# Kernel optimization log

Hardware: AMD Instinct MI355X
Metric: run time of the kernel (lower is better)

The kernel has to match this reference:

```python
import jax, jax.numpy as jnp
import numpy as np

N, H, W, SD = 64, 22, 22, 8
HW = H * W


def _conv(x, w, b):
    # 3x3 SAME conv, NCHW / OIHW
    y = jax.lax.conv_general_dilated(x, w, (1, 1), 'SAME',
                                     dimension_numbers=('NCHW', 'OIHW', 'NCHW'))
    return y + b[None, :, None, None]


def _bn(x, g, b, eps=1e-5):
    # BatchNorm2d in training mode: batch statistics over (N, H, W)
    m = jnp.mean(x, axis=(0, 2, 3), keepdims=True)
    v = jnp.var(x, axis=(0, 2, 3), keepdims=True)
    return (x - m) * jax.lax.rsqrt(v + eps) * g[None, :, None, None] + b[None, :, None, None]


def setup_inputs() -> dict:
    key = jax.random.key(0)
    ks = iter(jax.random.split(key, 64))
    def kw(shape):  # kaiming-normal fan_in init
        fan_in = int(np.prod(shape[1:]))
        return jax.random.normal(next(ks), shape, jnp.float32) * np.float32(np.sqrt(2.0 / fan_in))
    d = {
        'cost_volume': jax.random.normal(next(ks), (N, HW, H, W), jnp.float32),
        'state_prev': jax.random.normal(next(ks), (N, SD, H, W), jnp.float32),
        'dimp_score_cur': jax.random.normal(next(ks), (N, 1, H, W), jnp.float32),
    }
    for p in ('cv1', 'cv2'):  # two cost-volume processing stacks: conv(1->8)+BN+ReLU, conv(8->1)+BN
        d[p + '_w1'] = kw((8, 1, 3, 3)); d[p + '_b1'] = jnp.zeros(8, jnp.float32)
        d[p + '_g1'] = jnp.ones(8, jnp.float32); d[p + '_be1'] = jnp.zeros(8, jnp.float32)
        d[p + '_w2'] = kw((1, 8, 3, 3)); d[p + '_b2'] = jnp.zeros(1, jnp.float32)
        d[p + '_g2'] = jnp.ones(1, jnp.float32); d[p + '_be2'] = jnp.zeros(1, jnp.float32)
    d['rp1_w'] = kw((64, SD + 2, 3, 3)); d['rp1_b'] = jnp.zeros(64, jnp.float32)
    d['rp2_w'] = kw((32, 64, 3, 3)); d['rp2_b'] = jnp.zeros(32, jnp.float32)
    d['resp_w'] = kw((1, 32, 3, 3)); d['resp_b'] = jnp.zeros(1, jnp.float32)
    for g_ in ('gru_r', 'gru_u', 'gru_o'):  # ConvGRUCell(input=4, hidden=SD, ksz=3)
        d[g_ + 'w'] = kw((SD, 4 + SD, 3, 3)); d[g_ + 'b'] = jnp.zeros(SD, jnp.float32)
    return d


def _fwd(cost_volume, state_prev, dimp_score_cur,
         cv1_w1, cv1_b1, cv1_g1, cv1_be1, cv1_w2, cv1_b2, cv1_g2, cv1_be2,
         cv2_w1, cv2_b1, cv2_g1, cv2_be1, cv2_w2, cv2_b2, cv2_g2, cv2_be2,
         rp1_w, rp1_b, rp2_w, rp2_b, resp_w, resp_b,
         gru_rw, gru_rb, gru_uw, gru_ub, gru_ow, gru_ob):
    n = cost_volume.shape[0]
    # ---- cost volume processing 1: per-map spatial softmax ----
    x = cost_volume.reshape(-1, 1, H, W)                       # (N*HW, 1, H, W)
    p = jax.nn.relu(_bn(_conv(x, cv1_w1, cv1_b1), cv1_g1, cv1_be1))
    p = _bn(_conv(p, cv1_w2, cv1_b2), cv1_g2, cv1_be2)
    p = jax.nn.softmax(p.reshape(-1, HW), axis=1).reshape(-1, 1, H, W)
    # ---- cost volume processing 2: softmax over source positions ----
    p = jax.nn.relu(_bn(_conv(p, cv2_w1, cv2_b1), cv2_g1, cv2_be1))
    p = _bn(_conv(p, cv2_w2, cv2_b2), cv2_g2, cv2_be2)
    p = jax.nn.softmax(p.reshape(n, HW, H, W), axis=1)         # propagation weights (n, p, h, w)
    # ---- confidence ('max') ----
    conf = jnp.max(p, axis=1, keepdims=True)                   # (N, 1, H, W)
    # ---- state propagation: contract over source positions (no (N,HW,C,H,W) intermediate) ----
    s = state_prev.transpose(0, 2, 3, 1).reshape(n, HW, SD)    # (n, p, d)
    prop_h = jnp.einsum('nphw,npd->ndhw', p, s)                # (N, SD, H, W)
    # ---- response prediction ----
    pin = jnp.concatenate([prop_h, dimp_score_cur, conf], axis=1)   # (N, SD+2, H, W)
    r = jax.nn.relu(_conv(pin, rp1_w, rp1_b))
    r = jax.nn.relu(_conv(r, rp2_w, rp2_b))
    fused = jax.nn.sigmoid(_conv(r, resp_w, resp_b))           # (N, 1, H, W)
    # ---- ConvGRU state update ----
    scores_cat = jnp.concatenate([dimp_score_cur, fused], axis=1)   # (N, 2, H, W)
    pool = jnp.max(scores_cat, axis=(2, 3), keepdims=True)          # adaptive max pool to 1x1
    gin = jnp.concatenate([scores_cat, jnp.broadcast_to(pool, scores_cat.shape)], axis=1)  # (N,4,H,W)
    stacked = jnp.concatenate([gin, prop_h], axis=1)           # (N, 4+SD, H, W)
    upd = jax.nn.sigmoid(_conv(stacked, gru_uw, gru_ub))
    rst = jax.nn.sigmoid(_conv(stacked, gru_rw, gru_rb))
    out = jnp.tanh(_conv(jnp.concatenate([gin, prop_h * rst], axis=1), gru_ow, gru_ob))
    state_new = prop_h * (1.0 - upd) + out * upd               # (N, SD, H, W)
    return jnp.concatenate([fused, state_new], axis=1)         # (N, 1+SD, H, W)


def reference(cost_volume, state_prev, dimp_score_cur,
              cv1_w1, cv1_b1, cv1_g1, cv1_be1, cv1_w2, cv1_b2, cv1_g2, cv1_be2,
              cv2_w1, cv2_b1, cv2_g1, cv2_be1, cv2_w2, cv2_b2, cv2_g2, cv2_be2,
              rp1_w, rp1_b, rp2_w, rp2_b, resp_w, resp_b,
              gru_rw, gru_rb, gru_uw, gru_ub, gru_ow, gru_ob):
    return _fwd(cost_volume, state_prev, dimp_score_cur,
                cv1_w1, cv1_b1, cv1_g1, cv1_be1, cv1_w2, cv1_b2, cv1_g2, cv1_be2,
                cv2_w1, cv2_b1, cv2_g1, cv2_be1, cv2_w2, cv2_b2, cv2_g2, cv2_be2,
                rp1_w, rp1_b, rp2_w, rp2_b, resp_w, resp_b,
                gru_rw, gru_rb, gru_uw, gru_ub, gru_ow, gru_ob)
```

## Files before the change

kernel.cpp:

```cpp
#include <hip/hip_runtime.h>

#define HH 22
#define WW 22
#define HWN 484
#define NBATCH 64
#define SDIM 8
#define NMAPS (NBATCH*HWN)
#define PADW 24
#define PADSZ (PADW*PADW)
#define INVC (1.f/14992384.f)

#define LD12(A,b0) \
    float t00=(A)[(b0)],        t01=(A)[(b0)+1],        t02=(A)[(b0)+2], \
          t10=(A)[(b0)+PADW],   t11=(A)[(b0)+PADW+1],   t12=(A)[(b0)+PADW+2], \
          t20=(A)[(b0)+2*PADW], t21=(A)[(b0)+2*PADW+1], t22=(A)[(b0)+2*PADW+2], \
          t30=(A)[(b0)+3*PADW], t31=(A)[(b0)+3*PADW+1], t32=(A)[(b0)+3*PADW+2]

#define DOT9(w9,a0,a1,a2,b0_,b1_,b2_,c0,c1,c2,init) \
    fmaf((w9)[0],a0,fmaf((w9)[1],a1,fmaf((w9)[2],a2, \
    fmaf((w9)[3],b0_,fmaf((w9)[4],b1_,fmaf((w9)[5],b2_, \
    fmaf((w9)[6],c0,fmaf((w9)[7],c1,fmaf((w9)[8],c2,(init))))))))))

#define LOAD_NB(arr, bb) do { \
    nb[0]=(arr)[(bb)-PADW-1]; nb[1]=(arr)[(bb)-PADW]; nb[2]=(arr)[(bb)-PADW+1]; \
    nb[3]=(arr)[(bb)-1];      nb[4]=(arr)[(bb)];      nb[5]=(arr)[(bb)+1]; \
    nb[6]=(arr)[(bb)+PADW-1]; nb[7]=(arr)[(bb)+PADW]; nb[8]=(arr)[(bb)+PADW+1]; } while(0)

__global__ __launch_bounds__(256) void k_stats(const float* __restrict__ src,
    const float* __restrict__ w, const float* __restrict__ b,
    float* __restrict__ Sg, float* __restrict__ Qg)
{
    __shared__ float xin[PADSZ];
    __shared__ float red[16];
    int tid=threadIdx.x;
    for(int q=tid;q<PADSZ;q+=256) xin[q]=0.f;
    float accS[8], accQ[8];
#pragma unroll
    for(int c=0;c<8;++c){ accS[c]=0.f; accQ[c]=0.f; }
    bool act = tid<242;
    int i2 = tid/22, jj = tid - i2*22;
    int b0 = 2*i2*PADW + jj;
    int m0=blockIdx.x*16;
    for(int m=m0;m<m0+16;++m){
        __syncthreads();
        const float* sp = src + (size_t)m*HWN;
        { int p=tid;     int i=p/22, j=p-i*22; xin[(i+1)*PADW+j+1]=sp[p]; }
        { int p=tid+256; if(p<HWN){ int i=p/22, j=p-i*22; xin[(i+1)*PADW+j+1]=sp[p]; } }
        __syncthreads();
        if(act){
            LD12(xin,b0);
#pragma unroll
            for(int c=0;c<8;++c){
                const float* w9=w+c*9;
                float bc=b[c];
                float y0=DOT9(w9,t00,t01,t02,t10,t11,t12,t20,t21,t22,bc);
                float y1=DOT9(w9,t10,t11,t12,t20,t21,t22,t30,t31,t32,bc);
                accS[c]+=y0+y1;
                accQ[c]=fmaf(y0,y0,accQ[c]); accQ[c]=fmaf(y1,y1,accQ[c]);
            }
        }
    }
    __syncthreads();
    if(tid<16) red[tid]=0.f;
    __syncthreads();
#pragma unroll
    for(int c=0;c<8;++c){
        float s=accS[c], q=accQ[c];
        for(int o=32;o;o>>=1){ s+=__shfl_down(s,o); q+=__shfl_down(q,o); }
        if((tid&63)==0){ atomicAdd(&red[c],s); atomicAdd(&red[8+c],q); }
    }
    __syncthreads();
    if(tid<8){ atomicAdd(&Sg[tid],red[tid]); atomicAdd(&Qg[tid],red[8+tid]); }
}

__global__ __launch_bounds__(256) void k_convpair(const float* __restrict__ src, float* __restrict__ Ydst,
    const float* __restrict__ w1, const float* __restrict__ b1,
    const float* __restrict__ Sin, const float* __restrict__ Qin,
    const float* __restrict__ g, const float* __restrict__ be,
    const float* __restrict__ w2, const float* __restrict__ b2,
    float* __restrict__ Sg, float* __restrict__ Qg)
{
    __shared__ float xin[PADSZ];
    __shared__ float z[8*PADSZ];
    __shared__ float red[2];
    __shared__ float scs[8], shs[8];
    int tid=threadIdx.x;
    if(tid<8){
        float mean=Sin[tid]*INVC;
        float var=fmaf(-mean,mean,Qin[tid]*INVC);
        float sc=g[tid]*rsqrtf(var+1e-5f);
        scs[tid]=sc; shs[tid]=fmaf(-mean,sc,be[tid]);
    }
    for(int q=tid;q<PADSZ;q+=256) xin[q]=0.f;
    for(int q=tid;q<8*PADSZ;q+=256) z[q]=0.f;
    float aS=0.f, aQ=0.f;
    bool act = tid<242;
    int i2 = tid/22, jj = tid - i2*22;
    int b0 = 2*i2*PADW + jj;
    int zb = b0 + PADW + 1;
    int ptop = 2*i2*22 + jj;
    float b2v=b2[0];
    int m0=blockIdx.x*16;
    for(int m=m0;m<m0+16;++m){
        __syncthreads();
        const float* sp = src + (size_t)m*HWN;
        { int p=tid;     int i=p/22, j=p-i*22; xin[(i+1)*PADW+j+1]=sp[p]; }
        { int p=tid+256; if(p<HWN){ int i=p/22, j=p-i*22; xin[(i+1)*PADW+j+1]=sp[p]; } }
        __syncthreads();
        if(act){
            LD12(xin,b0);
#pragma unroll
            for(int c=0;c<8;++c){
                const float* w9=w1+c*9;
                float bc=b1[c], sc=scs[c], sh=shs[c];
                float y0=DOT9(w9,t00,t01,t02,t10,t11,t12,t20,t21,t22,bc);
                float y1=DOT9(w9,t10,t11,t12,t20,t21,t22,t30,t31,t32,bc);
                y0=fmaf(y0,sc,sh); y1=fmaf(y1,sc,sh);
                z[c*PADSZ+zb]      = y0>0.f?y0:0.f;
                z[c*PADSZ+zb+PADW] = y1>0.f?y1:0.f;
            }
        }
        __syncthreads();
        if(act){
            float y0=b2v, y1=b2v;
#pragma unroll
            for(int c=0;c<8;++c){
                const float* w9=w2+c*9;
                int cb=c*PADSZ+b0;
                LD12(z,cb);
                y0=DOT9(w9,t00,t01,t02,t10,t11,t12,t20,t21,t22,y0);
                y1=DOT9(w9,t10,t11,t12,t20,t21,t22,t30,t31,t32,y1);
            }
            float* yp = Ydst + (size_t)m*HWN;
            yp[ptop]=y0; yp[ptop+22]=y1;
            aS+=y0+y1; aQ=fmaf(y0,y0,aQ); aQ=fmaf(y1,y1,aQ);
        }
    }
    __syncthreads();
    if(tid<2) red[tid]=0.f;
    __syncthreads();
    for(int o=32;o;o>>=1){ aS+=__shfl_down(aS,o); aQ+=__shfl_down(aQ,o); }
    if((tid&63)==0){ atomicAdd(&red[0],aS); atomicAdd(&red[1],aQ); }
    __syncthreads();
    if(tid==0){ atomicAdd(Sg,red[0]); atomicAdd(Qg,red[1]); }
}

__global__ __launch_bounds__(256) void k_smax_stats(float* __restrict__ Y,
    const float* __restrict__ S2, const float* __restrict__ Q2,
    const float* __restrict__ g2, const float* __restrict__ be2,
    const float* __restrict__ w, const float* __restrict__ b,
    float* __restrict__ Sg, float* __restrict__ Qg)
{
    __shared__ float xin[PADSZ];
    __shared__ float red4[4];
    __shared__ float red[16];
    int tid=threadIdx.x;
    float mean=S2[0]*INVC;
    float var=fmaf(-mean,mean,Q2[0]*INVC);
    float a=g2[0]*rsqrtf(var+1e-5f);
    float sh=fmaf(-mean,a,be2[0]);
    for(int q=tid;q<PADSZ;q+=256) xin[q]=0.f;
    float accS[8], accQ[8];
#pragma unroll
    for(int c=0;c<8;++c){ accS[c]=0.f; accQ[c]=0.f; }
    bool act = tid<242;
    int i2 = tid/22, jj = tid - i2*22;
    int b0 = 2*i2*PADW + jj;
    int p0=tid, p1=tid+256;
    int i0=p0/22, j0=p0-i0*22; int aa0=(i0+1)*PADW+j0+1;
    int aa1=0; if(p1<HWN){ int i1=p1/22, j1=p1-i1*22; aa1=(i1+1)*PADW+j1+1; }
    int m0=blockIdx.x*16;
    for(int m=m0;m<m0+16;++m){
        __syncthreads();
        float* yp = Y + (size_t)m*HWN;
        float e0=__expf(fmaf(yp[p0],a,sh)); xin[aa0]=e0;
        float e1=0.f;
        if(p1<HWN){ e1=__expf(fmaf(yp[p1],a,sh)); xin[aa1]=e1; }
        float part=e0+e1;
        for(int o=32;o;o>>=1) part+=__shfl_down(part,o);
        if((tid&63)==0) red4[tid>>6]=part;
        __syncthreads();
        float inv=1.f/(red4[0]+red4[1]+red4[2]+red4[3]);
        yp[p0]=e0*inv;
        if(p1<HWN) yp[p1]=e1*inv;
        if(act){
            LD12(xin,b0);
#pragma unroll
            for(int c=0;c<8;++c){
                const float* w9=w+c*9;
                float d0=DOT9(w9,t00,t01,t02,t10,t11,t12,t20,t21,t22,0.f);
                float d1=DOT9(w9,t10,t11,t12,t20,t21,t22,t30,t31,t32,0.f);
                float y0=fmaf(inv,d0,b[c]);
                float y1=fmaf(inv,d1,b[c]);
                accS[c]+=y0+y1;
                accQ[c]=fmaf(y0,y0,accQ[c]); accQ[c]=fmaf(y1,y1,accQ[c]);
            }
        }
    }
    __syncthreads();
    if(tid<16) red[tid]=0.f;
    __syncthreads();
#pragma unroll
    for(int c=0;c<8;++c){
        float s=accS[c], q=accQ[c];
        for(int o=32;o;o>>=1){ s+=__shfl_down(s,o); q+=__shfl_down(q,o); }
        if((tid&63)==0){ atomicAdd(&red[c],s); atomicAdd(&red[8+c],q); }
    }
    __syncthreads();
    if(tid<8){ atomicAdd(&Sg[tid],red[tid]); atomicAdd(&Qg[tid],red[8+tid]); }
}

__global__ __launch_bounds__(128) void k_prop(const float* __restrict__ Y,
    const float* __restrict__ S4, const float* __restrict__ Q4,
    const float* __restrict__ g4, const float* __restrict__ be4,
    const float* __restrict__ state, float* __restrict__ prop, float* __restrict__ conf)
{
    int n=blockIdx.x;
    __shared__ float sst[8*HWN];
    int tid=threadIdx.x;
    for(int q=tid;q<8*HWN;q+=128) sst[q]=state[(size_t)n*8*HWN + q];
    __syncthreads();
    int t = blockIdx.y*121 + tid;
    if(tid>=121) return;
    float mean=S4[0]*INVC;
    float var=fmaf(-mean,mean,Q4[0]*INVC);
    float a=g4[0]*rsqrtf(var+1e-5f);
    float sh=fmaf(-mean,a,be4[0]);
    const float* col = Y + (size_t)n*HWN*HWN + t;
    float mx=-1e30f, ssum=0.f;
    float acc[8];
#pragma unroll
    for(int d=0;d<8;++d) acc[d]=0.f;
#pragma unroll 4
    for(int p=0;p<HWN;++p){
        float v=fmaf(col[(size_t)p*HWN], a, sh);
        float e=__expf(v);
        mx=fmaxf(mx,v);
        ssum+=e;
#pragma unroll
        for(int d=0;d<8;++d) acc[d]=fmaf(e, sst[d*HWN+p], acc[d]);
    }
    float inv=1.f/ssum;
    conf[(size_t)n*HWN+t]=__expf(mx)*inv;
#pragma unroll
    for(int d=0;d<8;++d) prop[((size_t)n*8+d)*HWN+t]=acc[d]*inv;
}

__global__ __launch_bounds__(256) void k_rp1(const float* __restrict__ prop,
    const float* __restrict__ dimp, const float* __restrict__ conf,
    const float* __restrict__ wf, const float* __restrict__ bfv, float* __restrict__ R1)
{
    int n=blockIdx.x, g=blockIdx.y;
    __shared__ float pin[10*PADSZ];
    int tid=threadIdx.x;
    for(int i=tid;i<10*PADSZ;i+=256) pin[i]=0.f;
    __syncthreads();
    for(int p=tid;p<HWN;p+=256){
        int i=p/WW, j=p-i*WW; int aa=(i+1)*PADW+j+1;
#pragma unroll
        for(int d=0;d<8;++d) pin[d*PADSZ+aa]=prop[((size_t)n*8+d)*HWN+p];
        pin[8*PADSZ+aa]=dimp[(size_t)n*HWN+p];
        pin[9*PADSZ+aa]=conf[(size_t)n*HWN+p];
    }
    __syncthreads();
    const float* wg = wf + (size_t)(g*16)*90;
    for(int p=tid;p<HWN;p+=256){
        int i=p/WW, j=p-i*WW; int aa=(i+1)*PADW+j+1;
        float acc[16];
#pragma unroll
        for(int o=0;o<16;++o) acc[o]=bfv[g*16+o];
#pragma unroll
        for(int c=0;c<10;++c){
            float nb[9]; int bb=c*PADSZ+aa;
            LOAD_NB(pin, bb);
#pragma unroll
            for(int o=0;o<16;++o){
                const float* w=wg+o*90+c*9;
#pragma unroll
                for(int t=0;t<9;++t) acc[o]=fmaf(w[t], nb[t], acc[o]);
            }
        }
#pragma unroll
        for(int o=0;o<16;++o){
            float y=acc[o];
            R1[((size_t)n*64 + g*16+o)*HWN+p]= y>0.f?y:0.f;
        }
    }
}

__global__ __launch_bounds__(512) void k_rp2(const float* __restrict__ R1,
    const float* __restrict__ wf, const float* __restrict__ bfv, float* __restrict__ R2)
{
    int n=blockIdx.x, g=blockIdx.y;
    __shared__ float xc[16*PADSZ];
    int tid=threadIdx.x;
    for(int i=tid;i<16*PADSZ;i+=512) xc[i]=0.f;
    int p=tid; bool act = p<HWN;
    int i=p/WW, j=p-i*WW, aa=(i+1)*PADW+j+1;
    float acc[8];
#pragma unroll
    for(int o=0;o<8;++o) acc[o]=0.f;
    for(int k=0;k<4;++k){
        __syncthreads();
        for(int q=tid;q<16*HWN;q+=512){
            int ic=q/HWN, pp=q-ic*HWN;
            int ii=pp/WW, jj=pp-ii*WW;
            xc[ic*PADSZ+(ii+1)*PADW+jj+1]=R1[((size_t)n*64 + k*16+ic)*HWN+pp];
        }
        __syncthreads();
        if(act){
#pragma unroll
            for(int ic=0;ic<16;++ic){
                float nb[9]; int bb=ic*PADSZ+aa;
                LOAD_NB(xc, bb);
#pragma unroll
                for(int o=0;o<8;++o){
                    const float* w = wf + ((size_t)(g*8+o)*64 + k*16+ic)*9;
#pragma unroll
                    for(int t=0;t<9;++t) acc[o]=fmaf(w[t], nb[t], acc[o]);
                }
            }
        }
    }
    if(act){
#pragma unroll
        for(int o=0;o<8;++o){
            float y=acc[o]+bfv[g*8+o];
            R2[((size_t)n*32+g*8+o)*HWN+p]= y>0.f?y:0.f;
        }
    }
}

__global__ __launch_bounds__(512) void k_resp(const float* __restrict__ R2,
    const float* __restrict__ wf, const float* __restrict__ bfv,
    const float* __restrict__ dimp, float* __restrict__ fused,
    float* __restrict__ pool, float* __restrict__ out)
{
    int n=blockIdx.x;
    __shared__ float xc[16*PADSZ];
    __shared__ float redf[8], redd[8];
    int tid=threadIdx.x;
    for(int i=tid;i<16*PADSZ;i+=512) xc[i]=0.f;
    int p=tid; bool act=p<HWN;
    int i=p/WW, j=p-i*WW, aa=(i+1)*PADW+j+1;
    float acc=0.f;
    for(int k=0;k<2;++k){
        __syncthreads();
        for(int q=tid;q<16*HWN;q+=512){
            int ic=q/HWN, pp=q-ic*HWN;
            int ii=pp/WW, jj=pp-ii*WW;
            xc[ic*PADSZ+(ii+1)*PADW+jj+1]=R2[((size_t)n*32+k*16+ic)*HWN+pp];
        }
        __syncthreads();
        if(act){
#pragma unroll
            for(int ic=0;ic<16;++ic){
                float nb[9]; int bb=ic*PADSZ+aa;
                LOAD_NB(xc, bb);
                const float* w=wf+(size_t)(k*16+ic)*9;
#pragma unroll
                for(int t=0;t<9;++t) acc=fmaf(w[t], nb[t], acc);
            }
        }
    }
    float fval=-1e30f, dval=-1e30f;
    if(act){
        float y=acc+bfv[0];
        float s=1.f/(1.f+__expf(-y));
        fused[(size_t)n*HWN+p]=s;
        out[(size_t)n*9*HWN+p]=s;
        fval=s;
        dval=dimp[(size_t)n*HWN+p];
    }
    int lane=tid&63, wid=tid>>6;
    for(int o=32;o;o>>=1){ fval=fmaxf(fval,__shfl_xor(fval,o)); dval=fmaxf(dval,__shfl_xor(dval,o)); }
    if(lane==0){ redf[wid]=fval; redd[wid]=dval; }
    __syncthreads();
    if(tid==0){
        float fm=redf[0], dm=redd[0];
        for(int q=1;q<8;++q){ fm=fmaxf(fm,redf[q]); dm=fmaxf(dm,redd[q]); }
        pool[n*2+0]=dm; pool[n*2+1]=fm;
    }
}

__global__ __launch_bounds__(512) void k_gru(const float* __restrict__ dimp,
    const float* __restrict__ fused, const float* __restrict__ pool,
    const float* __restrict__ prop,
    const float* __restrict__ wr, const float* __restrict__ br,
    const float* __restrict__ wu, const float* __restrict__ bu,
    const float* __restrict__ wo, const float* __restrict__ bo,
    float* __restrict__ out)
{
    int n=blockIdx.x;
    __shared__ float sg[12*PADSZ];
    __shared__ float pr[8*PADSZ];
    int tid=threadIdx.x;
    for(int i=tid;i<12*PADSZ;i+=512) sg[i]=0.f;
    for(int i=tid;i<8*PADSZ;i+=512) pr[i]=0.f;
    __syncthreads();
    float p0=pool[n*2+0], p1=pool[n*2+1];
    for(int p=tid;p<HWN;p+=512){
        int i=p/WW, j=p-i*WW, aa=(i+1)*PADW+j+1;
        sg[0*PADSZ+aa]=dimp[(size_t)n*HWN+p];
        sg[1*PADSZ+aa]=fused[(size_t)n*HWN+p];
        sg[2*PADSZ+aa]=p0;
        sg[3*PADSZ+aa]=p1;
#pragma unroll
        for(int d=0;d<8;++d) sg[(4+d)*PADSZ+aa]=prop[((size_t)n*8+d)*HWN+p];
    }
    __syncthreads();
    int p=tid; bool act=p<HWN;
    int i=p/WW, j=p-i*WW, aa=(i+1)*PADW+j+1;
    float upd[8];
    if(act){
        float ua[8], ra[8];
#pragma unroll
        for(int o=0;o<8;++o){ ua[o]=bu[o]; ra[o]=br[o]; }
#pragma unroll
        for(int ic=0;ic<12;++ic){
            float nb[9]; int bb=ic*PADSZ+aa;
            LOAD_NB(sg, bb);
#pragma unroll
            for(int o=0;o<8;++o){
                const float* wup=wu+((size_t)o*12+ic)*9;
                const float* wrp=wr+((size_t)o*12+ic)*9;
#pragma unroll
                for(int t=0;t<9;++t){
                    ua[o]=fmaf(wup[t], nb[t], ua[o]);
                    ra[o]=fmaf(wrp[t], nb[t], ra[o]);
                }
            }
        }
#pragma unroll
        for(int o=0;o<8;++o){
            upd[o]=1.f/(1.f+__expf(-ua[o]));
            float rst=1.f/(1.f+__expf(-ra[o]));
            pr[o*PADSZ+aa]=sg[(4+o)*PADSZ+aa]*rst;
        }
    }
    __syncthreads();
    if(act){
        float oa[8];
#pragma unroll
        for(int o=0;o<8;++o) oa[o]=bo[o];
#pragma unroll
        for(int ic=0;ic<12;++ic){
            const float* srcp = (ic<4)? (sg+ic*PADSZ) : (pr+(ic-4)*PADSZ);
            float nb[9]; int bb=aa;
            LOAD_NB(srcp, bb);
#pragma unroll
            for(int o=0;o<8;++o){
                const float* wop=wo+((size_t)o*12+ic)*9;
#pragma unroll
                for(int t=0;t<9;++t) oa[o]=fmaf(wop[t], nb[t], oa[o]);
            }
        }
#pragma unroll
        for(int o=0;o<8;++o){
            float od=tanhf(oa[o]);
            float ph=sg[(4+o)*PADSZ+aa];
            float sn=ph*(1.f-upd[o])+od*upd[o];
            out[((size_t)n*9+1+o)*HWN+p]=sn;
        }
    }
}

extern "C" void kernel_launch(void* const* d_in, const int* in_sizes, int n_in,
                              void* d_out, int out_size, void* d_ws, size_t ws_size,
                              hipStream_t stream)
{
    (void)in_sizes; (void)n_in; (void)out_size; (void)ws_size;
    float* ws=(float*)d_ws;
    float* Y     = ws;
    float* PROP  = ws + 14992384;
    float* CONF  = PROP + 247808;
    float* FUSED = CONF + 30976;
    float* POOL  = FUSED + 30976;
    float* STATS = POOL + 128;
    float* R1    = ws;
    float* R2    = ws + 4000000;

    const float* cv    = (const float*)d_in[0];
    const float* state = (const float*)d_in[1];
    const float* dimp  = (const float*)d_in[2];
    float* out = (float*)d_out;

    hipMemsetAsync(STATS, 0, 36*sizeof(float), stream);

    float *S1=STATS,*Q1=STATS+8,*S2=STATS+16,*Q2=STATS+17,*S3=STATS+18,*Q3=STATS+26,*S4=STATS+34,*Q4=STATS+35;

    const float* cv1_w1=(const float*)d_in[3];  const float* cv1_b1=(const float*)d_in[4];
    const float* cv1_g1=(const float*)d_in[5];  const float* cv1_be1=(const float*)d_in[6];
    const float* cv1_w2=(const float*)d_in[7];  const float* cv1_b2=(const float*)d_in[8];
    const float* cv1_g2=(const float*)d_in[9];  const float* cv1_be2=(const float*)d_in[10];
    const float* cv2_w1=(const float*)d_in[11]; const float* cv2_b1=(const float*)d_in[12];
    const float* cv2_g1=(const float*)d_in[13]; const float* cv2_be1=(const float*)d_in[14];
    const float* cv2_w2=(const float*)d_in[15]; const float* cv2_b2=(const float*)d_in[16];
    const float* cv2_g2=(const float*)d_in[17]; const float* cv2_be2=(const float*)d_in[18];
    const float* rp1_w=(const float*)d_in[19];  const float* rp1_b=(const float*)d_in[20];
    const float* rp2_w=(const float*)d_in[21];  const float* rp2_b=(const float*)d_in[22];
    const float* resp_w=(const float*)d_in[23]; const float* resp_b=(const float*)d_in[24];
    const float* gru_rw=(const float*)d_in[25]; const float* gru_rb=(const float*)d_in[26];
    const float* gru_uw=(const float*)d_in[27]; const float* gru_ub=(const float*)d_in[28];
    const float* gru_ow=(const float*)d_in[29]; const float* gru_ob=(const float*)d_in[30];

    k_stats<<<1936,256,0,stream>>>(cv, cv1_w1, cv1_b1, S1, Q1);
    k_convpair<<<1936,256,0,stream>>>(cv, Y, cv1_w1, cv1_b1, S1, Q1, cv1_g1, cv1_be1,
                                      cv1_w2, cv1_b2, S2, Q2);
    k_smax_stats<<<1936,256,0,stream>>>(Y, S2, Q2, cv1_g2, cv1_be2, cv2_w1, cv2_b1, S3, Q3);
    k_convpair<<<1936,256,0,stream>>>(Y, Y, cv2_w1, cv2_b1, S3, Q3, cv2_g1, cv2_be1,
                                      cv2_w2, cv2_b2, S4, Q4);
    k_prop<<<dim3(64,4),128,0,stream>>>(Y, S4, Q4, cv2_g2, cv2_be2, state, PROP, CONF);
    k_rp1<<<dim3(64,4),256,0,stream>>>(PROP, dimp, CONF, rp1_w, rp1_b, R1);
    k_rp2<<<dim3(64,4),512,0,stream>>>(R1, rp2_w, rp2_b, R2);
    k_resp<<<64,512,0,stream>>>(R2, resp_w, resp_b, dimp, FUSED, POOL, out);
    k_gru<<<64,512,0,stream>>>(dimp, FUSED, POOL, PROP,
                               gru_rw, gru_rb, gru_uw, gru_ub, gru_ow, gru_ob, out);
}
```

Baseline: 849.4 us.

## Map one thread per padded cell, double-buffer map loads, split prop reduction

```diff
diff --git a/kernel.cpp b/kernel.cpp
--- a/kernel.cpp
+++ b/kernel.cpp
@@ -6,61 +6,57 @@
 #define NBATCH 64
 #define SDIM 8
 #define NMAPS (NBATCH*HWN)
+#define PW 24
+#define CELLS 576
 #define PADW 24
 #define PADSZ (PADW*PADW)
 #define INVC (1.f/14992384.f)
 
-#define LD12(A,b0) \
-    float t00=(A)[(b0)],        t01=(A)[(b0)+1],        t02=(A)[(b0)+2], \
-          t10=(A)[(b0)+PADW],   t11=(A)[(b0)+PADW+1],   t12=(A)[(b0)+PADW+2], \
-          t20=(A)[(b0)+2*PADW], t21=(A)[(b0)+2*PADW+1], t22=(A)[(b0)+2*PADW+2], \
-          t30=(A)[(b0)+3*PADW], t31=(A)[(b0)+3*PADW+1], t32=(A)[(b0)+3*PADW+2]
-
-#define DOT9(w9,a0,a1,a2,b0_,b1_,b2_,c0,c1,c2,init) \
-    fmaf((w9)[0],a0,fmaf((w9)[1],a1,fmaf((w9)[2],a2, \
-    fmaf((w9)[3],b0_,fmaf((w9)[4],b1_,fmaf((w9)[5],b2_, \
-    fmaf((w9)[6],c0,fmaf((w9)[7],c1,fmaf((w9)[8],c2,(init))))))))))
+#define LD9(A, idx) \
+  float x0=(A)[(idx)-PW-1], x1=(A)[(idx)-PW], x2=(A)[(idx)-PW+1], \
+        x3=(A)[(idx)-1],    x4=(A)[(idx)],    x5=(A)[(idx)+1], \
+        x6=(A)[(idx)+PW-1], x7=(A)[(idx)+PW], x8=(A)[(idx)+PW+1]
+#define DOT9W(w9, init) \
+  fmaf((w9)[0],x0,fmaf((w9)[1],x1,fmaf((w9)[2],x2,fmaf((w9)[3],x3,fmaf((w9)[4],x4, \
+  fmaf((w9)[5],x5,fmaf((w9)[6],x6,fmaf((w9)[7],x7,fmaf((w9)[8],x8,(init))))))))))
 
 #define LOAD_NB(arr, bb) do { \
     nb[0]=(arr)[(bb)-PADW-1]; nb[1]=(arr)[(bb)-PADW]; nb[2]=(arr)[(bb)-PADW+1]; \
     nb[3]=(arr)[(bb)-1];      nb[4]=(arr)[(bb)];      nb[5]=(arr)[(bb)+1]; \
     nb[6]=(arr)[(bb)+PADW-1]; nb[7]=(arr)[(bb)+PADW]; nb[8]=(arr)[(bb)+PADW+1]; } while(0)
 
-__global__ __launch_bounds__(256) void k_stats(const float* __restrict__ src,
+__global__ __launch_bounds__(576) void k_stats(const float* __restrict__ src,
     const float* __restrict__ w, const float* __restrict__ b,
     float* __restrict__ Sg, float* __restrict__ Qg)
 {
-    __shared__ float xin[PADSZ];
+    __shared__ float xin[2][CELLS];
     __shared__ float red[16];
     int tid=threadIdx.x;
-    for(int q=tid;q<PADSZ;q+=256) xin[q]=0.f;
+    int i=tid/PW, j=tid-i*PW;
+    bool inter = (i>=1 && i<=22 && j>=1 && j<=22);
+    int p=(i-1)*22+(j-1);
+    xin[0][tid]=0.f; xin[1][tid]=0.f;
     float accS[8], accQ[8];
 #pragma unroll
     for(int c=0;c<8;++c){ accS[c]=0.f; accQ[c]=0.f; }
-    bool act = tid<242;
-    int i2 = tid/22, jj = tid - i2*22;
-    int b0 = 2*i2*PADW + jj;
     int m0=blockIdx.x*16;
-    for(int m=m0;m<m0+16;++m){
-        __syncthreads();
-        const float* sp = src + (size_t)m*HWN;
-        { int p=tid;     int i=p/22, j=p-i*22; xin[(i+1)*PADW+j+1]=sp[p]; }
-        { int p=tid+256; if(p<HWN){ int i=p/22, j=p-i*22; xin[(i+1)*PADW+j+1]=sp[p]; } }
-        __syncthreads();
-        if(act){
-            LD12(xin,b0);
+    if(inter) xin[0][tid]=src[(size_t)m0*HWN+p];
+    __syncthreads();
+    for(int mi=0;mi<16;++mi){
+        int cur=mi&1;
+        float nx=0.f;
+        if(mi<15 && inter) nx=src[(size_t)(m0+mi+1)*HWN+p];
+        if(inter){
+            LD9(xin[cur], tid);
 #pragma unroll
             for(int c=0;c<8;++c){
-                const float* w9=w+c*9;
-                float bc=b[c];
-                float y0=DOT9(w9,t00,t01,t02,t10,t11,t12,t20,t21,t22,bc);
-                float y1=DOT9(w9,t10,t11,t12,t20,t21,t22,t30,t31,t32,bc);
-                accS[c]+=y0+y1;
-                accQ[c]=fmaf(y0,y0,accQ[c]); accQ[c]=fmaf(y1,y1,accQ[c]);
-            }
-        }
-    }
-    __syncthreads();
+                float y=DOT9W(w+c*9, b[c]);
+                accS[c]+=y; accQ[c]=fmaf(y,y,accQ[c]);
+            }
+        }
+        if(mi<15 && inter) xin[cur^1][tid]=nx;
+        __syncthreads();
+    }
     if(tid<16) red[tid]=0.f;
     __syncthreads();
 #pragma unroll
@@ -73,70 +69,62 @@
     if(tid<8){ atomicAdd(&Sg[tid],red[tid]); atomicAdd(&Qg[tid],red[8+tid]); }
 }
 
-__global__ __launch_bounds__(256) void k_convpair(const float* __restrict__ src, float* __restrict__ Ydst,
+__global__ __launch_bounds__(576) void k_convpair(const float* __restrict__ src, float* __restrict__ Ydst,
     const float* __restrict__ w1, const float* __restrict__ b1,
     const float* __restrict__ Sin, const float* __restrict__ Qin,
     const float* __restrict__ g, const float* __restrict__ be,
     const float* __restrict__ w2, const float* __restrict__ b2,
     float* __restrict__ Sg, float* __restrict__ Qg)
 {
-    __shared__ float xin[PADSZ];
-    __shared__ float z[8*PADSZ];
+    __shared__ float xin[2][CELLS];
+    __shared__ float z[8][CELLS];
+    __shared__ float scs[8], shs[8];
     __shared__ float red[2];
-    __shared__ float scs[8], shs[8];
-    int tid=threadIdx.x;
+    int tid=threadIdx.x;
+    int i=tid/PW, j=tid-i*PW;
+    bool inter = (i>=1 && i<=22 && j>=1 && j<=22);
+    int p=(i-1)*22+(j-1);
+    xin[0][tid]=0.f; xin[1][tid]=0.f;
+#pragma unroll
+    for(int c=0;c<8;++c) z[c][tid]=0.f;
     if(tid<8){
         float mean=Sin[tid]*INVC;
         float var=fmaf(-mean,mean,Qin[tid]*INVC);
         float sc=g[tid]*rsqrtf(var+1e-5f);
         scs[tid]=sc; shs[tid]=fmaf(-mean,sc,be[tid]);
     }
-    for(int q=tid;q<PADSZ;q+=256) xin[q]=0.f;
-    for(int q=tid;q<8*PADSZ;q+=256) z[q]=0.f;
     float aS=0.f, aQ=0.f;
-    bool act = tid<242;
-    int i2 = tid/22, jj = tid - i2*22;
-    int b0 = 2*i2*PADW + jj;
-    int zb = b0 + PADW + 1;
-    int ptop = 2*i2*22 + jj;
     float b2v=b2[0];
     int m0=blockIdx.x*16;
-    for(int m=m0;m<m0+16;++m){
-        __syncthreads();
-        const float* sp = src + (size_t)m*HWN;
-        { int p=tid;     int i=p/22, j=p-i*22; xin[(i+1)*PADW+j+1]=sp[p]; }
-        { int p=tid+256; if(p<HWN){ int i=p/22, j=p-i*22; xin[(i+1)*PADW+j+1]=sp[p]; } }
-        __syncthreads();
-        if(act){
-            LD12(xin,b0);
+    if(inter) xin[0][tid]=src[(size_t)m0*HWN+p];
+    __syncthreads();
+    for(int mi=0;mi<16;++mi){
+        int cur=mi&1;
+        float nx=0.f;
+        if(mi<15 && inter) nx=src[(size_t)(m0+mi+1)*HWN+p];
+        if(inter){
+            LD9(xin[cur], tid);
 #pragma unroll
             for(int c=0;c<8;++c){
-                const float* w9=w1+c*9;
-                float bc=b1[c], sc=scs[c], sh=shs[c];
-                float y0=DOT9(w9,t00,t01,t02,t10,t11,t12,t20,t21,t22,bc);
-                float y1=DOT9(w9,t10,t11,t12,t20,t21,t22,t30,t31,t32,bc);
-                y0=fmaf(y0,sc,sh); y1=fmaf(y1,sc,sh);
-                z[c*PADSZ+zb]      = y0>0.f?y0:0.f;
-                z[c*PADSZ+zb+PADW] = y1>0.f?y1:0.f;
-            }
-        }
-        __syncthreads();
-        if(act){
-            float y0=b2v, y1=b2v;
+                float y=DOT9W(w1+c*9, b1[c]);
+                y=fmaf(y,scs[c],shs[c]);
+                z[c][tid]=y>0.f?y:0.f;
+            }
+        }
+        if(mi<15 && inter) xin[cur^1][tid]=nx;
+        __syncthreads();
+        if(inter){
+            float y=b2v;
 #pragma unroll
             for(int c=0;c<8;++c){
-                const float* w9=w2+c*9;
-                int cb=c*PADSZ+b0;
-                LD12(z,cb);
-                y0=DOT9(w9,t00,t01,t02,t10,t11,t12,t20,t21,t22,y0);
-                y1=DOT9(w9,t10,t11,t12,t20,t21,t22,t30,t31,t32,y1);
-            }
-            float* yp = Ydst + (size_t)m*HWN;
-            yp[ptop]=y0; yp[ptop+22]=y1;
-            aS+=y0+y1; aQ=fmaf(y0,y0,aQ); aQ=fmaf(y1,y1,aQ);
-        }
-    }
-    __syncthreads();
+                LD9(z[c], tid);
+                y=DOT9W(w2+c*9, y);
+            }
+            Ydst[(size_t)(m0+mi)*HWN+p]=y;
+            aS+=y; aQ=fmaf(y,y,aQ);
+        }
+        __syncthreads();
+    }
     if(tid<2) red[tid]=0.f;
     __syncthreads();
     for(int o=32;o;o>>=1){ aS+=__shfl_down(aS,o); aQ+=__shfl_down(aQ,o); }
@@ -145,59 +133,50 @@
     if(tid==0){ atomicAdd(Sg,red[0]); atomicAdd(Qg,red[1]); }
 }
 
-__global__ __launch_bounds__(256) void k_smax_stats(float* __restrict__ Y,
+__global__ __launch_bounds__(576) void k_smax_stats(float* __restrict__ Y,
     const float* __restrict__ S2, const float* __restrict__ Q2,
     const float* __restrict__ g2, const float* __restrict__ be2,
     const float* __restrict__ w, const float* __restrict__ b,
     float* __restrict__ Sg, float* __restrict__ Qg)
 {
-    __shared__ float xin[PADSZ];
-    __shared__ float red4[4];
+    __shared__ float xin[CELLS];
+    __shared__ float red9[9];
     __shared__ float red[16];
     int tid=threadIdx.x;
+    int i=tid/PW, j=tid-i*PW;
+    bool inter = (i>=1 && i<=22 && j>=1 && j<=22);
+    int p=(i-1)*22+(j-1);
     float mean=S2[0]*INVC;
     float var=fmaf(-mean,mean,Q2[0]*INVC);
     float a=g2[0]*rsqrtf(var+1e-5f);
     float sh=fmaf(-mean,a,be2[0]);
-    for(int q=tid;q<PADSZ;q+=256) xin[q]=0.f;
+    xin[tid]=0.f;
     float accS[8], accQ[8];
 #pragma unroll
     for(int c=0;c<8;++c){ accS[c]=0.f; accQ[c]=0.f; }
-    bool act = tid<242;
-    int i2 = tid/22, jj = tid - i2*22;
-    int b0 = 2*i2*PADW + jj;
-    int p0=tid, p1=tid+256;
-    int i0=p0/22, j0=p0-i0*22; int aa0=(i0+1)*PADW+j0+1;
-    int aa1=0; if(p1<HWN){ int i1=p1/22, j1=p1-i1*22; aa1=(i1+1)*PADW+j1+1; }
     int m0=blockIdx.x*16;
-    for(int m=m0;m<m0+16;++m){
-        __syncthreads();
-        float* yp = Y + (size_t)m*HWN;
-        float e0=__expf(fmaf(yp[p0],a,sh)); xin[aa0]=e0;
-        float e1=0.f;
-        if(p1<HWN){ e1=__expf(fmaf(yp[p1],a,sh)); xin[aa1]=e1; }
-        float part=e0+e1;
+    for(int mi=0;mi<16;++mi){
+        size_t off=(size_t)(m0+mi)*HWN+p;
+        float e = inter ? __expf(fmaf(Y[off],a,sh)) : 0.f;
+        float part=e;
         for(int o=32;o;o>>=1) part+=__shfl_down(part,o);
-        if((tid&63)==0) red4[tid>>6]=part;
-        __syncthreads();
-        float inv=1.f/(red4[0]+red4[1]+red4[2]+red4[3]);
-        yp[p0]=e0*inv;
-        if(p1<HWN) yp[p1]=e1*inv;
-        if(act){
-            LD12(xin,b0);
+        if((tid&63)==0) red9[tid>>6]=part;
+        xin[tid]=e;
+        __syncthreads();
+        float sum=red9[0]+red9[1]+red9[2]+red9[3]+red9[4]+red9[5]+red9[6]+red9[7]+red9[8];
+        float inv=1.f/sum;
+        if(inter){
+            Y[off]=e*inv;
+            LD9(xin, tid);
 #pragma unroll
             for(int c=0;c<8;++c){
-                const float* w9=w+c*9;
-                float d0=DOT9(w9,t00,t01,t02,t10,t11,t12,t20,t21,t22,0.f);
-                float d1=DOT9(w9,t10,t11,t12,t20,t21,t22,t30,t31,t32,0.f);
-                float y0=fmaf(inv,d0,b[c]);
-                float y1=fmaf(inv,d1,b[c]);
-                accS[c]+=y0+y1;
-                accQ[c]=fmaf(y0,y0,accQ[c]); accQ[c]=fmaf(y1,y1,accQ[c]);
-            }
-        }
-    }
-    __syncthreads();
+                float d=DOT9W(w+c*9, 0.f);
+                float y=fmaf(inv,d,b[c]);
+                accS[c]+=y; accQ[c]=fmaf(y,y,accQ[c]);
+            }
+        }
+        __syncthreads();
+    }
     if(tid<16) red[tid]=0.f;
     __syncthreads();
 #pragma unroll
@@ -210,40 +189,54 @@
     if(tid<8){ atomicAdd(&Sg[tid],red[tid]); atomicAdd(&Qg[tid],red[8+tid]); }
 }
 
-__global__ __launch_bounds__(128) void k_prop(const float* __restrict__ Y,
+__global__ __launch_bounds__(512) void k_prop(const float* __restrict__ Y,
     const float* __restrict__ S4, const float* __restrict__ Q4,
     const float* __restrict__ g4, const float* __restrict__ be4,
     const float* __restrict__ state, float* __restrict__ prop, float* __restrict__ conf)
 {
     int n=blockIdx.x;
     __shared__ float sst[8*HWN];
-    int tid=threadIdx.x;
-    for(int q=tid;q<8*HWN;q+=128) sst[q]=state[(size_t)n*8*HWN + q];
-    __syncthreads();
-    int t = blockIdx.y*121 + tid;
-    if(tid>=121) return;
+    __shared__ float part[4][121][10];
+    int tid=threadIdx.x;
+    for(int q=tid;q<8*HWN;q+=512) sst[q]=state[(size_t)n*8*HWN + q];
+    __syncthreads();
+    int tq=tid&127, pc=tid>>7;
+    int t=blockIdx.y*121+tq;
     float mean=S4[0]*INVC;
     float var=fmaf(-mean,mean,Q4[0]*INVC);
     float a=g4[0]*rsqrtf(var+1e-5f);
     float sh=fmaf(-mean,a,be4[0]);
-    const float* col = Y + (size_t)n*HWN*HWN + t;
-    float mx=-1e30f, ssum=0.f;
-    float acc[8];
-#pragma unroll
-    for(int d=0;d<8;++d) acc[d]=0.f;
+    if(tq<121){
+        const float* col = Y + (size_t)n*HWN*HWN + t + (size_t)pc*121*HWN;
+        const float* sp = sst + pc*121;
+        float mx=-1e30f, ssum=0.f;
+        float acc[8];
+#pragma unroll
+        for(int d=0;d<8;++d) acc[d]=0.f;
 #pragma unroll 4
-    for(int p=0;p<HWN;++p){
-        float v=fmaf(col[(size_t)p*HWN], a, sh);
-        float e=__expf(v);
-        mx=fmaxf(mx,v);
-        ssum+=e;
-#pragma unroll
-        for(int d=0;d<8;++d) acc[d]=fmaf(e, sst[d*HWN+p], acc[d]);
-    }
-    float inv=1.f/ssum;
-    conf[(size_t)n*HWN+t]=__expf(mx)*inv;
-#pragma unroll
-    for(int d=0;d<8;++d) prop[((size_t)n*8+d)*HWN+t]=acc[d]*inv;
+        for(int p=0;p<121;++p){
+            float v=fmaf(col[(size_t)p*HWN], a, sh);
+            float e=__expf(v);
+            mx=fmaxf(mx,v); ssum+=e;
+#pragma unroll
+            for(int d=0;d<8;++d) acc[d]=fmaf(e, sp[d*HWN+p], acc[d]);
+        }
+        part[pc][tq][0]=ssum; part[pc][tq][1]=mx;
+#pragma unroll
+        for(int d=0;d<8;++d) part[pc][tq][2+d]=acc[d];
+    }
+    __syncthreads();
+    if(pc==0 && tq<121){
+        float ssum=part[0][tq][0]+part[1][tq][0]+part[2][tq][0]+part[3][tq][0];
+        float mx=fmaxf(fmaxf(part[0][tq][1],part[1][tq][1]),fmaxf(part[2][tq][1],part[3][tq][1]));
+        float inv=1.f/ssum;
+        conf[(size_t)n*HWN+t]=__expf(mx)*inv;
+#pragma unroll
+        for(int d=0;d<8;++d){
+            float acd=part[0][tq][2+d]+part[1][tq][2+d]+part[2][tq][2+d]+part[3][tq][2+d];
+            prop[((size_t)n*8+d)*HWN+t]=acd*inv;
+        }
+    }
 }
 
 __global__ __launch_bounds__(256) void k_rp1(const float* __restrict__ prop,
@@ -504,13 +497,13 @@
     const float* gru_uw=(const float*)d_in[27]; const float* gru_ub=(const float*)d_in[28];
     const float* gru_ow=(const float*)d_in[29]; const float* gru_ob=(const float*)d_in[30];
 
-    k_stats<<<1936,256,0,stream>>>(cv, cv1_w1, cv1_b1, S1, Q1);
-    k_convpair<<<1936,256,0,stream>>>(cv, Y, cv1_w1, cv1_b1, S1, Q1, cv1_g1, cv1_be1,
+    k_stats<<<1936,576,0,stream>>>(cv, cv1_w1, cv1_b1, S1, Q1);
+    k_convpair<<<1936,576,0,stream>>>(cv, Y, cv1_w1, cv1_b1, S1, Q1, cv1_g1, cv1_be1,
                                       cv1_w2, cv1_b2, S2, Q2);
-    k_smax_stats<<<1936,256,0,stream>>>(Y, S2, Q2, cv1_g2, cv1_be2, cv2_w1, cv2_b1, S3, Q3);
-    k_convpair<<<1936,256,0,stream>>>(Y, Y, cv2_w1, cv2_b1, S3, Q3, cv2_g1, cv2_be1,
+    k_smax_stats<<<1936,576,0,stream>>>(Y, S2, Q2, cv1_g2, cv1_be2, cv2_w1, cv2_b1, S3, Q3);
+    k_convpair<<<1936,576,0,stream>>>(Y, Y, cv2_w1, cv2_b1, S3, Q3, cv2_g1, cv2_be1,
                                       cv2_w2, cv2_b2, S4, Q4);
-    k_prop<<<dim3(64,4),128,0,stream>>>(Y, S4, Q4, cv2_g2, cv2_be2, state, PROP, CONF);
+    k_prop<<<dim3(64,4),512,0,stream>>>(Y, S4, Q4, cv2_g2, cv2_be2, state, PROP, CONF);
     k_rp1<<<dim3(64,4),256,0,stream>>>(PROP, dimp, CONF, rp1_w, rp1_b, R1);
     k_rp2<<<dim3(64,4),512,0,stream>>>(R1, rp2_w, rp2_b, R2);
     k_resp<<<64,512,0,stream>>>(R2, resp_w, resp_b, dimp, FUSED, POOL, out);
```

Measured after the change: 969.7 us. 1.14x slower.
